# Performance work log

Measured on AMD Instinct MI355X. Metric: run time of the kernel, lower is better.

The kernel has to match this reference:

```python
import jax, jax.numpy as jnp
import numpy as np

NUM_GRAPHS = 8
NEG_SLOPE = 0.2


def add_self_loops(edge_index, n):
    loops = jnp.arange(n, dtype=edge_index.dtype)
    src = jnp.concatenate([edge_index[0], loops])
    dst = jnp.concatenate([edge_index[1], loops])
    return src, dst


def gat_conv(x, src, dst, W, att_src, att_dst, bias, concat):
    # x: [N, F_in]; W: [F_in, H*C]; att_src/att_dst: [H, C]; bias: [H*C] or [C]
    n = x.shape[0]
    H, C = att_src.shape
    xl = (x @ W).reshape(n, H, C)                     # [N, H, C]
    a_src = jnp.einsum('nhc,hc->nh', xl, att_src)     # [N, H]
    a_dst = jnp.einsum('nhc,hc->nh', xl, att_dst)     # [N, H]
    e = jax.nn.leaky_relu(a_src[src] + a_dst[dst], NEG_SLOPE)  # [E, H]
    # segment softmax over edges grouped by destination node
    m = jax.ops.segment_max(e, dst, num_segments=n)   # [N, H]
    e = jnp.exp(e - m[dst])
    denom = jax.ops.segment_sum(e, dst, num_segments=n)
    alpha = e / (denom[dst] + 1e-16)                  # [E, H]
    msg = xl[src] * alpha[:, :, None]                 # [E, H, C]
    out = jax.ops.segment_sum(msg, dst, num_segments=n)  # [N, H, C]
    out = out.reshape(n, H * C) if concat else out.mean(axis=1)
    return out + bias


def global_mean_pool(x, batch, num_graphs):
    s = jax.ops.segment_sum(x, batch, num_segments=num_graphs)
    cnt = jax.ops.segment_sum(jnp.ones((x.shape[0],), x.dtype), batch, num_segments=num_graphs)
    return s / jnp.maximum(cnt, 1.0)[:, None]


def setup_inputs() -> dict:
    key = jax.random.key(0)
    ks = jax.random.split(key, 12)
    N, E, F_in, Ch, H, F_out = 50000, 800000, 128, 64, 4, 128
    x = jax.random.normal(ks[0], (N, F_in), dtype=jnp.float32)
    edge_index = jax.random.randint(ks[1], (2, E), 0, N, dtype=jnp.int64)
    batch = jnp.sort(jax.random.randint(ks[2], (N,), 0, NUM_GRAPHS, dtype=jnp.int64))
    s = 0.1
    W1 = jax.random.normal(ks[3], (F_in, H * Ch), dtype=jnp.float32) * s
    att_src1 = jax.random.normal(ks[4], (H, Ch), dtype=jnp.float32) * s
    att_dst1 = jax.random.normal(ks[5], (H, Ch), dtype=jnp.float32) * s
    bias1 = jnp.zeros((H * Ch,), dtype=jnp.float32)
    W2 = jax.random.normal(ks[6], (H * Ch, F_out), dtype=jnp.float32) * s
    att_src2 = jax.random.normal(ks[7], (1, F_out), dtype=jnp.float32) * s
    att_dst2 = jax.random.normal(ks[8], (1, F_out), dtype=jnp.float32) * s
    bias2 = jnp.zeros((F_out,), dtype=jnp.float32)
    return {"x": x, "edge_index": edge_index, "batch": batch,
            "W1": W1, "att_src1": att_src1, "att_dst1": att_dst1, "bias1": bias1,
            "W2": W2, "att_src2": att_src2, "att_dst2": att_dst2, "bias2": bias2}


def reference(x, edge_index, batch, W1, att_src1, att_dst1, bias1, W2, att_src2, att_dst2, bias2):
    n = x.shape[0]
    src, dst = add_self_loops(edge_index, n)
    h = gat_conv(x, src, dst, W1, att_src1, att_dst1, bias1, concat=True)
    h = jax.nn.relu(h)
    h = gat_conv(h, src, dst, W2, att_src2, att_dst2, bias2, concat=False)
    return global_mean_pool(h, batch, NUM_GRAPHS)
```

## Files before the change

kernel.cpp:

```cpp
#include <hip/hip_runtime.h>
#include <cstdint>
#include <cstddef>

#define NEG_SLOPE 0.2f
#define LOG2E 1.44269504088896f
#define NREP 64

typedef __attribute__((ext_vector_type(8))) short bf16x8;
typedef __attribute__((ext_vector_type(4))) float f32x4;
typedef __attribute__((ext_vector_type(2))) float f32x2;

__device__ __forceinline__ ushort f2b(float f) {
  unsigned u = __float_as_uint(f);
  return (ushort)((u + 0x7FFFu + ((u >> 16) & 1)) >> 16);
}
__device__ __forceinline__ float fexp2(float x) {
#if __has_builtin(__builtin_amdgcn_exp2f)
  return __builtin_amdgcn_exp2f(x);
#else
  return __exp2f(x);
#endif
}
__device__ __forceinline__ int lbound(const int* __restrict__ a, int n, int key) {
  int lo = 0, hi = n;
  while (lo < hi) { int m = (lo + hi) >> 1; if (a[m] < key) lo = m + 1; else hi = m; }
  return lo;
}

__global__ __launch_bounds__(256) void setup_k(const float* __restrict__ W1,
                                               ushort* __restrict__ Bp1,
                                               const float* __restrict__ W2,
                                               ushort* __restrict__ Bp2,
                                               int* __restrict__ hist,
                                               float* __restrict__ pp, int n) {
  int i = blockIdx.x * 256 + threadIdx.x;
  {
    int k = i >> 8, c = i & 255;
    Bp1[(((size_t)(k >> 3) * 256 + c) << 3) + (k & 7)] = f2b(W1[i]);
  }
  {
    int k = i >> 7, c = i & 127;
    Bp2[(((size_t)(k >> 3) * 128 + c) << 3) + (k & 7)] = f2b(W2[i]);
  }
  if (i < n) hist[i] = 0;
  int i2 = i + 32768;
  if (i2 < n) hist[i2] = 0;
  pp[i] = 0.f;
  pp[i + 32768] = 0.f;
}

template<int N, int K, int C, int H, bool AF32>
__device__ __forceinline__ void gemm_attn_body(const void* __restrict__ A_,
                                               const ushort* __restrict__ Bp,
                                               const float* __restrict__ att_src,
                                               const float* __restrict__ att_dst,
                                               unsigned char* __restrict__ C8,
                                               float* __restrict__ a_src,
                                               float* __restrict__ a_dst,
                                               int M, int bid) {
  const int wave = threadIdx.x >> 6;
  const int lane = threadIdx.x & 63;
  const int strips = M / 16;
  const int strip = bid * 4 + wave;
  if (strip >= strips) return;
  const int r = lane & 15, kg = lane >> 4;
  const int row = strip * 16 + r;

  bf16x8 a[K / 32];
  if constexpr (AF32) {
    const float* Af = (const float*)A_;
    #pragma unroll
    for (int k0 = 0; k0 < K / 32; ++k0) {
      float4 f0 = *(const float4*)(Af + (size_t)row * K + k0 * 32 + kg * 8);
      float4 f1 = *(const float4*)(Af + (size_t)row * K + k0 * 32 + kg * 8 + 4);
      bf16x8 t;
      t[0] = (short)f2b(f0.x); t[1] = (short)f2b(f0.y);
      t[2] = (short)f2b(f0.z); t[3] = (short)f2b(f0.w);
      t[4] = (short)f2b(f1.x); t[5] = (short)f2b(f1.y);
      t[6] = (short)f2b(f1.z); t[7] = (short)f2b(f1.w);
      a[k0] = t;
    }
  } else {
    const ushort* Ab = (const ushort*)A_;
    #pragma unroll
    for (int k0 = 0; k0 < K / 32; ++k0)
      a[k0] = *(const bf16x8*)(Ab + (size_t)row * K + k0 * 32 + kg * 8);
  }

  float as_part[4] = {}, ad_part[4] = {};
  #pragma unroll 2
  for (int n0 = 0; n0 < N / 16; ++n0) {
    f32x4 acc = {0.f, 0.f, 0.f, 0.f};
    #pragma unroll
    for (int k0 = 0; k0 < K / 32; ++k0) {
      bf16x8 b = *(const bf16x8*)(Bp + ((size_t)(k0 * 4 + kg) * N + n0 * 16 + r) * 8);
      acc = __builtin_amdgcn_mfma_f32_16x16x32_bf16(a[k0], b, acc, 0, 0, 0);
    }
    float asv = att_src[n0 * 16 + r] * LOG2E;
    float adv = att_dst[n0 * 16 + r] * LOG2E;
    #pragma unroll
    for (int i = 0; i < 4; ++i) {
      as_part[i] = fmaf(acc[i], asv, as_part[i]);
      ad_part[i] = fmaf(acc[i], adv, ad_part[i]);
    }
    #pragma unroll
    for (int i = 0; i < 4; ++i) {
      int pk = __builtin_amdgcn_cvt_pk_fp8_f32(acc[i], acc[i], 0, false);
      C8[((size_t)strip * 16 + kg * 4 + i) * N + n0 * 16 + r] = (unsigned char)(pk & 0xFF);
    }
    if (((n0 + 1) * 16) % C == 0) {
      int h = (n0 * 16) / C;
      #pragma unroll
      for (int i = 0; i < 4; ++i) {
        float ts = as_part[i], td = ad_part[i];
        #pragma unroll
        for (int off = 1; off < 16; off <<= 1) {
          ts += __shfl_xor(ts, off);
          td += __shfl_xor(td, off);
        }
        if (r == i) {
          a_src[(size_t)(strip * 16 + kg * 4 + i) * H + h] = ts;
          a_dst[(size_t)(strip * 16 + kg * 4 + i) * H + h] = td;
        }
        as_part[i] = 0.f;
        ad_part[i] = 0.f;
      }
    }
  }
}

template<int N, int K, int C, int H, bool AF32>
__global__ __launch_bounds__(256) void gemm_rank_k(const void* __restrict__ A_,
                                                   const ushort* __restrict__ Bp,
                                                   const float* __restrict__ att_src,
                                                   const float* __restrict__ att_dst,
                                                   unsigned char* __restrict__ C8,
                                                   float* __restrict__ a_src,
                                                   float* __restrict__ a_dst, int M,
                                                   const int* __restrict__ edst,
                                                   int* __restrict__ hist,
                                                   int* __restrict__ rank,
                                                   int E, int GB) {
  if ((int)blockIdx.x < GB) {
    gemm_attn_body<N, K, C, H, AF32>(A_, Bp, att_src, att_dst, C8, a_src, a_dst,
                                     M, blockIdx.x);
  } else {
    int base = ((blockIdx.x - GB) * 256 + threadIdx.x) * 8;
    #pragma unroll
    for (int u = 0; u < 8; ++u) {
      int e = base + u;
      if (e < E) rank[e] = atomicAdd(hist + edst[e], 1);
    }
  }
}

template<int N, int K, int C, int H, bool AF32>
__global__ __launch_bounds__(256) void gemm_attn_k(const void* __restrict__ A_,
                                                   const ushort* __restrict__ Bp,
                                                   const float* __restrict__ att_src,
                                                   const float* __restrict__ att_dst,
                                                   unsigned char* __restrict__ C8,
                                                   float* __restrict__ a_src,
                                                   float* __restrict__ a_dst, int M) {
  gemm_attn_body<N, K, C, H, AF32>(A_, Bp, att_src, att_dst, C8, a_src, a_dst,
                                   M, blockIdx.x);
}

__global__ __launch_bounds__(256) void scan1_k(const int* __restrict__ hist,
                                               int* __restrict__ excl,
                                               int* __restrict__ chunksum, int n) {
  __shared__ int sums[256];
  int base = blockIdx.x * 1024 + threadIdx.x * 4;
  int4 v = {0, 0, 0, 0};
  if (base + 3 < n) v = *(const int4*)(hist + base);
  else {
    if (base < n)     v.x = hist[base];
    if (base + 1 < n) v.y = hist[base + 1];
    if (base + 2 < n) v.z = hist[base + 2];
    if (base + 3 < n) v.w = hist[base + 3];
  }
  int s = v.x + v.y + v.z + v.w;
  sums[threadIdx.x] = s;
  __syncthreads();
  for (int off = 1; off < 256; off <<= 1) {
    int t = (threadIdx.x >= (unsigned)off) ? sums[threadIdx.x - off] : 0;
    __syncthreads();
    sums[threadIdx.x] += t;
    __syncthreads();
  }
  if (threadIdx.x == 255) chunksum[blockIdx.x] = sums[255];
  int e0 = sums[threadIdx.x] - s;
  int e1 = e0 + v.x, e2 = e1 + v.y, e3 = e2 + v.z;
  if (base + 3 < n) {
    int4 o = {e0, e1, e2, e3};
    *(int4*)(excl + base) = o;
  } else {
    if (base < n)     excl[base] = e0;
    if (base + 1 < n) excl[base + 1] = e1;
    if (base + 2 < n) excl[base + 2] = e2;
    if (base + 3 < n) excl[base + 3] = e3;
  }
}

__global__ void scan2_k(const int* __restrict__ chunksum,
                        int* __restrict__ chunkoff, int nchunks) {
  if (threadIdx.x == 0) {
    int run = 0;
    for (int c = 0; c < nchunks; ++c) { chunkoff[c] = run; run += chunksum[c]; }
  }
}

__global__ __launch_bounds__(256) void addoff_k(int* __restrict__ rowptr,
                                                const int* __restrict__ chunkoff,
                                                int n, int total) {
  int i = blockIdx.x * 256 + threadIdx.x;
  if (i == 0) rowptr[n] = total;
  if (i >= n) return;
  rowptr[i] += chunkoff[i >> 10];
}

__global__ __launch_bounds__(256) void fill_k(const int* __restrict__ esrc,
                                              const int* __restrict__ edst,
                                              const int* __restrict__ rowptr,
                                              const int* __restrict__ rank,
                                              int* __restrict__ csr_src,
                                              int E, int Epad) {
  int e = blockIdx.x * 256 + threadIdx.x;
  if (e < E) csr_src[rowptr[edst[e]] + rank[e]] = esrc[e];
  else if (e < Epad) csr_src[e] = 0;
}

template<int H, int C>
__global__ __launch_bounds__(256) void agg1_k(const int* __restrict__ rowptr,
                                              const int* __restrict__ csr,
                                              const float* __restrict__ a_src,
                                              const float* __restrict__ a_dst,
                                              const unsigned char* __restrict__ xl,
                                              const float* __restrict__ bias,
                                              ushort* __restrict__ out, int n) {
  constexpr int F = H * C;
  const int wid0 = (blockIdx.x * 256 + threadIdx.x) >> 6;
  if (wid0 >= n) return;
  const int wid = __builtin_amdgcn_readfirstlane(wid0);
  const int lane = threadIdx.x & 63;
  const int h = lane >> 4;
  const uint lofs = (uint)lane * 4;
  const int j4 = lane & 3;
  const int je = lane >> 2;
  const int beg = rowptr[wid];
  const int end = rowptr[wid + 1];

  const float adh_s = a_dst[(uint)wid * 4 + j4];
  float vs_s = a_src[(uint)wid * 4 + j4] + adh_s;
  vs_s = fmaxf(vs_s, NEG_SLOPE * vs_s);

  float den = 1.f;
  float acc[4];
  {
    uint xs = *(const uint*)(xl + ((uint)wid * F + lofs));
    f32x2 lo = __builtin_amdgcn_cvt_pk_f32_fp8(xs, false);
    f32x2 hi = __builtin_amdgcn_cvt_pk_f32_fp8(xs, true);
    acc[0] = lo[0]; acc[1] = lo[1]; acc[2] = hi[0]; acc[3] = hi[1];
  }

  for (int j = beg; j < end; j += 16) {
    int sl = csr[j + je];
    float t = a_src[(uint)sl * 4 + j4] + adh_s;
    t = fmaxf(t, NEG_SLOPE * t);
    t = (j + je < end) ? t - vs_s : -1e30f;
    float pl = fexp2(t);
    uint xv[16];
    #pragma unroll
    for (int u = 0; u < 16; ++u) {
      int su = csr[j + u];
      xv[u] = *(const uint*)(xl + ((uint)su * F + lofs));
    }
    #pragma unroll
    for (int u = 0; u < 16; ++u) {
      float pu = __shfl(pl, u * 4 + h);
      den += pu;
      f32x2 lo = __builtin_amdgcn_cvt_pk_f32_fp8(xv[u], false);
      f32x2 hi = __builtin_amdgcn_cvt_pk_f32_fp8(xv[u], true);
      acc[0] = fmaf(pu, lo[0], acc[0]);
      acc[1] = fmaf(pu, lo[1], acc[1]);
      acc[2] = fmaf(pu, hi[0], acc[2]);
      acc[3] = fmaf(pu, hi[1], acc[3]);
    }
  }

  float inv = 1.f / (den + 1e-16f);
  float o[4];
  #pragma unroll
  for (int i = 0; i < 4; ++i)
    o[i] = fmaxf(fmaf(acc[i], inv, bias[lane * 4 + i]), 0.f);
  ushort4 ov = {f2b(o[0]), f2b(o[1]), f2b(o[2]), f2b(o[3])};
  *(ushort4*)(out + (size_t)wid * F + lane * 4) = ov;
}

__global__ __launch_bounds__(256) void agg2pool_k(const int* __restrict__ rowptr,
                                                  const int* __restrict__ csr,
                                                  const float* __restrict__ a_src,
                                                  const float* __restrict__ a_dst,
                                                  const unsigned char* __restrict__ xl,
                                                  const int* __restrict__ batch,
                                                  float* __restrict__ pp,
                                                  int n, int Emax) {
  const int pair = (blockIdx.x * 256 + threadIdx.x) >> 6;
  const int lane = threadIdx.x & 63;
  const int l32 = lane & 31;
  const int half = lane >> 5;
  int wid = pair * 2 + half;
  const bool act = wid < n;
  if (!act) wid = n - 1;
  const uint lofs = (uint)l32 * 4;
  const int beg = rowptr[wid];
  const int deg = rowptr[wid + 1] - beg;
  const int mdeg = max(deg, __shfl_xor(deg, 32));
  const float adh = a_dst[wid];

  float vs = a_src[wid] + adh;
  vs = fmaxf(vs, NEG_SLOPE * vs);
  float den = 1.f;
  float acc[4];
  {
    uint xs = *(const uint*)(xl + ((uint)wid * 128 + lofs));
    f32x2 lo = __builtin_amdgcn_cvt_pk_f32_fp8(xs, false);
    f32x2 hi = __builtin_amdgcn_cvt_pk_f32_fp8(xs, true);
    acc[0] = lo[0]; acc[1] = lo[1]; acc[2] = hi[0]; acc[3] = hi[1];
  }

  for (int j = 0; j < mdeg; j += 32) {
    int sl = csr[min(beg + j + l32, Emax)];
    float t = a_src[sl] + adh;
    t = fmaxf(t, NEG_SLOPE * t);
    t = (j + l32 < deg) ? t - vs : -1e30f;
    float pl = fexp2(t);
    #pragma unroll
    for (int g = 0; g < 2; ++g) {
      int su[16];
      uint xv[16];
      #pragma unroll
      for (int u = 0; u < 16; ++u) {
        su[u] = __shfl(sl, half * 32 + g * 16 + u);
        xv[u] = *(const uint*)(xl + ((uint)su[u] * 128 + lofs));
      }
      #pragma unroll
      for (int u = 0; u < 16; ++u) {
        float pu = __shfl(pl, half * 32 + g * 16 + u);
        den += pu;
        f32x2 lo = __builtin_amdgcn_cvt_pk_f32_fp8(xv[u], false);
        f32x2 hi = __builtin_amdgcn_cvt_pk_f32_fp8(xv[u], true);
        acc[0] = fmaf(pu, lo[0], acc[0]);
        acc[1] = fmaf(pu, lo[1], acc[1]);
        acc[2] = fmaf(pu, hi[0], acc[2]);
        acc[3] = fmaf(pu, hi[1], acc[3]);
      }
    }
  }

  __shared__ float red[8][128];
  __shared__ int gids[8];
  const int rrow = (threadIdx.x >> 6) * 2 + half;
  float inv = act ? 1.f / (den + 1e-16f) : 0.f;
  float4 ov = {acc[0] * inv, acc[1] * inv, acc[2] * inv, acc[3] * inv};
  *(float4*)&red[rrow][l32 * 4] = ov;
  if (l32 == 0) gids[rrow] = act ? batch[wid] : -1;
  __syncthreads();
  if (threadIdx.x < 128) {
    const int ch = threadIdx.x;
    float* base = pp + (size_t)(blockIdx.x & (NREP - 1)) * 8 * 128;
    float sum = 0.f;
    int cur = gids[0];
    #pragma unroll
    for (int r = 0; r < 8; ++r) {
      int g = gids[r];
      if (g != cur) {
        if (cur >= 0) unsafeAtomicAdd(base + cur * 128 + ch, sum);
        sum = 0.f;
        cur = g;
      }
      if (g >= 0) sum += red[r][ch];
    }
    if (cur >= 0) unsafeAtomicAdd(base + cur * 128 + ch, sum);
  }
}

__global__ __launch_bounds__(256) void finalize_k(const float* __restrict__ pp,
                                                  const int* __restrict__ batch,
                                                  const float* __restrict__ bias2,
                                                  float* __restrict__ out, int n) {
  int t = blockIdx.x * 256 + threadIdx.x;
  if (t >= 8 * 128) return;
  int g = t >> 7, c = t & 127;
  float s = 0.f;
  #pragma unroll 8
  for (int rep = 0; rep < NREP; ++rep) s += pp[rep * 8 * 128 + t];
  int lo = lbound(batch, n, g);
  int hi = lbound(batch, n, g + 1);
  float cnt = (float)(hi - lo);
  out[t] = s / fmaxf(cnt, 1.f) + bias2[c];
}

extern "C" void kernel_launch(void* const* d_in, const int* in_sizes, int n_in,
                              void* d_out, int out_size, void* d_ws, size_t ws_size,
                              hipStream_t stream) {
  const float* x        = (const float*)d_in[0];
  const int*   ei       = (const int*)d_in[1];
  const int*   batch    = (const int*)d_in[2];
  const float* W1       = (const float*)d_in[3];
  const float* att_src1 = (const float*)d_in[4];
  const float* att_dst1 = (const float*)d_in[5];
  const float* bias1    = (const float*)d_in[6];
  const float* W2       = (const float*)d_in[7];
  const float* att_src2 = (const float*)d_in[8];
  const float* att_dst2 = (const float*)d_in[9];
  const float* bias2    = (const float*)d_in[10];
  float* out = (float*)d_out;

  const int E  = in_sizes[1] / 2;
  const int NN = in_sizes[2];
  const int* esrc = ei;
  const int* edst = ei + E;
  const int PAD = 64;

  char* w = (char*)d_ws;
  size_t woff = 0;
  auto walloc = [&](size_t bytes) -> char* {
    char* r = w + woff;
    woff += (bytes + 255) & ~(size_t)255;
    return r;
  };
  unsigned char* xl1 = (unsigned char*)walloc((size_t)NN * 256);
  ushort* h1     = (ushort*)walloc((size_t)NN * 256 * 2);
  unsigned char* xl2 = (unsigned char*)walloc((size_t)NN * 128);
  float*  a_src1 = (float*)walloc((size_t)NN * 4 * 4);
  float*  a_dst1 = (float*)walloc((size_t)NN * 4 * 4);
  float*  a_src2 = (float*)walloc((size_t)NN * 4);
  float*  a_dst2 = (float*)walloc((size_t)NN * 4);
  int*    rowptr = (int*)walloc((size_t)(NN + 1) * 4);
  int*    hist   = (int*)walloc((size_t)NN * 4);
  int*    rank   = (int*)walloc((size_t)E * 4);
  int*    csrsrc = (int*)walloc((size_t)(E + PAD) * 4);
  ushort* Bp1    = (ushort*)walloc(128 * 256 * 2);
  ushort* Bp2    = (ushort*)walloc(256 * 128 * 2);
  int*    chunks = (int*)walloc(256 * 4);
  int*    chunko = (int*)walloc(256 * 4);
  float*  pp     = (float*)walloc((size_t)NREP * 8 * 128 * 4);

  dim3 blk(256);
  const int nbEp = (E + PAD + 255) / 256;
  const int nbN4 = (NN + 3) / 4;
  const int nbP  = ((NN + 1) / 2 + 3) / 4;
  const int gblocks = (NN / 16 + 3) / 4;
  const int rankBlocks = (E + 2047) / 2048;
  const int nchunks = (NN + 1023) / 1024;

  setup_k<<<128, blk, 0, stream>>>(W1, Bp1, W2, Bp2, hist, pp, NN);

  gemm_rank_k<256, 128, 64, 4, true><<<gblocks + rankBlocks, blk, 0, stream>>>(
      x, Bp1, att_src1, att_dst1, xl1, a_src1, a_dst1, NN,
      edst, hist, rank, E, gblocks);

  scan1_k<<<nchunks, blk, 0, stream>>>(hist, rowptr, chunks, NN);
  scan2_k<<<1, 64, 0, stream>>>(chunks, chunko, nchunks);
  addoff_k<<<(NN + 255) / 256, blk, 0, stream>>>(rowptr, chunko, NN, E);

  fill_k<<<nbEp, blk, 0, stream>>>(esrc, edst, rowptr, rank, csrsrc, E, E + PAD);

  agg1_k<4, 64><<<nbN4, blk, 0, stream>>>(
      rowptr, csrsrc, a_src1, a_dst1, xl1, bias1, h1, NN);

  gemm_attn_k<128, 256, 128, 1, false><<<gblocks, blk, 0, stream>>>(
      h1, Bp2, att_src2, att_dst2, xl2, a_src2, a_dst2, NN);

  agg2pool_k<<<nbP, blk, 0, stream>>>(
      rowptr, csrsrc, a_src2, a_dst2, xl2, batch, pp, NN, E + PAD - 1);

  finalize_k<<<4, blk, 0, stream>>>(pp, batch, bias2, out, NN);
}
```

Baseline: 162.3 us.

## Split GEMM column tiles across two waves and store FP8 output via LDS transpose

Each 16-row strip is now handled by two waves, each computing half of the output column tiles, which doubles the number of GEMM blocks. The FP8 results are transposed through shared memory so each lane writes a packed 4-byte word instead of single bytes. For layer 2 the two waves write partial attention logits, which the aggregation kernel reads as float2 and sums. The aim is more parallelism and fewer, wider stores, at the cost of extra LDS traffic and a doubled attention-logit buffer for layer 2.

```diff
diff --git a/kernel.cpp b/kernel.cpp
--- a/kernel.cpp
+++ b/kernel.cpp
@@ -49,7 +49,7 @@
   pp[i + 32768] = 0.f;
 }
 
-template<int N, int K, int C, int H, bool AF32>
+template<int N, int K, int C, int H, bool AF32, bool PARTIAL>
 __device__ __forceinline__ void gemm_attn_body(const void* __restrict__ A_,
                                                const ushort* __restrict__ Bp,
                                                const float* __restrict__ att_src,
@@ -58,13 +58,19 @@
                                                float* __restrict__ a_src,
                                                float* __restrict__ a_dst,
                                                int M, int bid) {
+  constexpr int T = N / 16;
+  constexpr int TH = T / 2;
+  __shared__ float tile[4][16][20];
   const int wave = threadIdx.x >> 6;
   const int lane = threadIdx.x & 63;
   const int strips = M / 16;
-  const int strip = bid * 4 + wave;
+  const int strip = bid * 2 + (wave >> 1);
+  const int half = wave & 1;
   if (strip >= strips) return;
   const int r = lane & 15, kg = lane >> 4;
   const int row = strip * 16 + r;
+  const int rt = kg * 4 + (r & 3);
+  const int cg = r >> 2;
 
   bf16x8 a[K / 32];
   if constexpr (AF32) {
@@ -88,8 +94,9 @@
   }
 
   float as_part[4] = {}, ad_part[4] = {};
-  #pragma unroll 2
-  for (int n0 = 0; n0 < N / 16; ++n0) {
+  #pragma unroll
+  for (int t = 0; t < TH; ++t) {
+    const int n0 = half * TH + t;
     f32x4 acc = {0.f, 0.f, 0.f, 0.f};
     #pragma unroll
     for (int k0 = 0; k0 < K / 32; ++k0) {
@@ -104,26 +111,46 @@
       ad_part[i] = fmaf(acc[i], adv, ad_part[i]);
     }
     #pragma unroll
+    for (int i = 0; i < 4; ++i) tile[wave][kg * 4 + i][r] = acc[i];
+    asm volatile("s_waitcnt lgkmcnt(0)" ::: "memory");
+    float4 tv = *(const float4*)&tile[wave][rt][cg * 4];
+    int dw = __builtin_amdgcn_cvt_pk_fp8_f32(tv.x, tv.y, 0, false);
+    dw = __builtin_amdgcn_cvt_pk_fp8_f32(tv.z, tv.w, dw, true);
+    *(unsigned*)(C8 + (size_t)(strip * 16 + rt) * N + (uint)(n0 * 16 + cg * 4)) =
+        (unsigned)dw;
+    if constexpr (!PARTIAL) {
+      if (((n0 + 1) * 16) % C == 0) {
+        int h = (n0 * 16) / C;
+        #pragma unroll
+        for (int i = 0; i < 4; ++i) {
+          float ts = as_part[i], td = ad_part[i];
+          #pragma unroll
+          for (int off = 1; off < 16; off <<= 1) {
+            ts += __shfl_xor(ts, off);
+            td += __shfl_xor(td, off);
+          }
+          if (r == i) {
+            a_src[(size_t)(strip * 16 + kg * 4 + i) * H + h] = ts;
+            a_dst[(size_t)(strip * 16 + kg * 4 + i) * H + h] = td;
+          }
+          as_part[i] = 0.f;
+          ad_part[i] = 0.f;
+        }
+      }
+    }
+  }
+  if constexpr (PARTIAL) {
+    #pragma unroll
     for (int i = 0; i < 4; ++i) {
-      int pk = __builtin_amdgcn_cvt_pk_fp8_f32(acc[i], acc[i], 0, false);
-      C8[((size_t)strip * 16 + kg * 4 + i) * N + n0 * 16 + r] = (unsigned char)(pk & 0xFF);
-    }
-    if (((n0 + 1) * 16) % C == 0) {
-      int h = (n0 * 16) / C;
+      float ts = as_part[i], td = ad_part[i];
       #pragma unroll
-      for (int i = 0; i < 4; ++i) {
-        float ts = as_part[i], td = ad_part[i];
-        #pragma unroll
-        for (int off = 1; off < 16; off <<= 1) {
-          ts += __shfl_xor(ts, off);
-          td += __shfl_xor(td, off);
-        }
-        if (r == i) {
-          a_src[(size_t)(strip * 16 + kg * 4 + i) * H + h] = ts;
-          a_dst[(size_t)(strip * 16 + kg * 4 + i) * H + h] = td;
-        }
-        as_part[i] = 0.f;
-        ad_part[i] = 0.f;
+      for (int off = 1; off < 16; off <<= 1) {
+        ts += __shfl_xor(ts, off);
+        td += __shfl_xor(td, off);
+      }
+      if (r == i) {
+        a_src[(size_t)(strip * 16 + kg * 4 + i) * 2 + half] = ts;
+        a_dst[(size_t)(strip * 16 + kg * 4 + i) * 2 + half] = td;
       }
     }
   }
@@ -142,8 +169,8 @@
                                                    int* __restrict__ rank,
                                                    int E, int GB) {
   if ((int)blockIdx.x < GB) {
-    gemm_attn_body<N, K, C, H, AF32>(A_, Bp, att_src, att_dst, C8, a_src, a_dst,
-                                     M, blockIdx.x);
+    gemm_attn_body<N, K, C, H, AF32, false>(A_, Bp, att_src, att_dst, C8,
+                                            a_src, a_dst, M, blockIdx.x);
   } else {
     int base = ((blockIdx.x - GB) * 256 + threadIdx.x) * 8;
     #pragma unroll
@@ -162,8 +189,8 @@
                                                    unsigned char* __restrict__ C8,
                                                    float* __restrict__ a_src,
                                                    float* __restrict__ a_dst, int M) {
-  gemm_attn_body<N, K, C, H, AF32>(A_, Bp, att_src, att_dst, C8, a_src, a_dst,
-                                   M, blockIdx.x);
+  gemm_attn_body<N, K, C, H, AF32, true>(A_, Bp, att_src, att_dst, C8,
+                                         a_src, a_dst, M, blockIdx.x);
 }
 
 __global__ __launch_bounds__(256) void scan1_k(const int* __restrict__ hist,
@@ -316,9 +343,11 @@
   const int beg = rowptr[wid];
   const int deg = rowptr[wid + 1] - beg;
   const int mdeg = max(deg, __shfl_xor(deg, 32));
-  const float adh = a_dst[wid];
-
-  float vs = a_src[wid] + adh;
+  const float2 ad2 = ((const float2*)a_dst)[wid];
+  const float adh = ad2.x + ad2.y;
+
+  float2 av2 = ((const float2*)a_src)[wid];
+  float vs = av2.x + av2.y + adh;
   vs = fmaxf(vs, NEG_SLOPE * vs);
   float den = 1.f;
   float acc[4];
@@ -331,7 +360,8 @@
 
   for (int j = 0; j < mdeg; j += 32) {
     int sl = csr[min(beg + j + l32, Emax)];
-    float t = a_src[sl] + adh;
+    float2 as2 = ((const float2*)a_src)[sl];
+    float t = as2.x + as2.y + adh;
     t = fmaxf(t, NEG_SLOPE * t);
     t = (j + l32 < deg) ? t - vs : -1e30f;
     float pl = fexp2(t);
@@ -435,8 +465,8 @@
   unsigned char* xl2 = (unsigned char*)walloc((size_t)NN * 128);
   float*  a_src1 = (float*)walloc((size_t)NN * 4 * 4);
   float*  a_dst1 = (float*)walloc((size_t)NN * 4 * 4);
-  float*  a_src2 = (float*)walloc((size_t)NN * 4);
-  float*  a_dst2 = (float*)walloc((size_t)NN * 4);
+  float*  a_src2 = (float*)walloc((size_t)NN * 2 * 4);
+  float*  a_dst2 = (float*)walloc((size_t)NN * 2 * 4);
   int*    rowptr = (int*)walloc((size_t)(NN + 1) * 4);
   int*    hist   = (int*)walloc((size_t)NN * 4);
   int*    rank   = (int*)walloc((size_t)E * 4);
@@ -451,7 +481,8 @@
   const int nbEp = (E + PAD + 255) / 256;
   const int nbN4 = (NN + 3) / 4;
   const int nbP  = ((NN + 1) / 2 + 3) / 4;
-  const int gblocks = (NN / 16 + 3) / 4;
+  const int strips = NN / 16;
+  const int gblocks = (strips * 2 + 3) / 4;
   const int rankBlocks = (E + 2047) / 2048;
   const int nchunks = (NN + 1023) / 1024;
 
```

After: 170.7 us. 5.2% more time.

## Stage packed weights in LDS and swap MFMA operands for row-contiguous output

Applied to the files above, without the earlier changes.

Each GEMM block now copies the packed bf16 weight matrix into shared memory with a rotation swizzle to avoid bank conflicts, and reads B fragments from LDS instead of global memory. The MFMA operands are swapped so each lane holds four consecutive output columns of one row. This lets the fp8 output be written as a packed 32-bit store and shortens the attention-score reduction to two cross-lane shuffles. The cost is 64 KB of shared memory per block, which limits occupancy, plus a full weight copy and a barrier in every block.

```diff
diff --git a/kernel.cpp b/kernel.cpp
--- a/kernel.cpp
+++ b/kernel.cpp
@@ -58,21 +58,33 @@
                                                float* __restrict__ a_src,
                                                float* __restrict__ a_dst,
                                                int M, int bid) {
-  const int wave = threadIdx.x >> 6;
-  const int lane = threadIdx.x & 63;
+  constexpr int ROWS = K / 8;
+  __shared__ ushort Bl[ROWS * N * 8];
+  const int tid = threadIdx.x;
+  #pragma unroll
+  for (int it = 0; it < ROWS * N / 256; ++it) {
+    int id = it * 256 + tid;
+    int brow = id / N, c = id % N;
+    int cs = (c + 2 * brow) & (N - 1);
+    *(bf16x8*)&Bl[((size_t)brow * N + cs) * 8] = *(const bf16x8*)&Bp[(size_t)id * 8];
+  }
+  __syncthreads();
+
+  const int wave = tid >> 6;
+  const int lane = tid & 63;
   const int strips = M / 16;
   const int strip = bid * 4 + wave;
   if (strip >= strips) return;
   const int r = lane & 15, kg = lane >> 4;
-  const int row = strip * 16 + r;
+  const int nrow = strip * 16 + r;
 
   bf16x8 a[K / 32];
   if constexpr (AF32) {
     const float* Af = (const float*)A_;
     #pragma unroll
     for (int k0 = 0; k0 < K / 32; ++k0) {
-      float4 f0 = *(const float4*)(Af + (size_t)row * K + k0 * 32 + kg * 8);
-      float4 f1 = *(const float4*)(Af + (size_t)row * K + k0 * 32 + kg * 8 + 4);
+      float4 f0 = *(const float4*)(Af + (size_t)nrow * K + k0 * 32 + kg * 8);
+      float4 f1 = *(const float4*)(Af + (size_t)nrow * K + k0 * 32 + kg * 8 + 4);
       bf16x8 t;
       t[0] = (short)f2b(f0.x); t[1] = (short)f2b(f0.y);
       t[2] = (short)f2b(f0.z); t[3] = (short)f2b(f0.w);
@@ -84,47 +96,37 @@
     const ushort* Ab = (const ushort*)A_;
     #pragma unroll
     for (int k0 = 0; k0 < K / 32; ++k0)
-      a[k0] = *(const bf16x8*)(Ab + (size_t)row * K + k0 * 32 + kg * 8);
-  }
-
-  float as_part[4] = {}, ad_part[4] = {};
-  #pragma unroll 2
+      a[k0] = *(const bf16x8*)(Ab + (size_t)nrow * K + k0 * 32 + kg * 8);
+  }
+
+  float as_p = 0.f, ad_p = 0.f;
+  #pragma unroll
   for (int n0 = 0; n0 < N / 16; ++n0) {
     f32x4 acc = {0.f, 0.f, 0.f, 0.f};
     #pragma unroll
     for (int k0 = 0; k0 < K / 32; ++k0) {
-      bf16x8 b = *(const bf16x8*)(Bp + ((size_t)(k0 * 4 + kg) * N + n0 * 16 + r) * 8);
-      acc = __builtin_amdgcn_mfma_f32_16x16x32_bf16(a[k0], b, acc, 0, 0, 0);
-    }
-    float asv = att_src[n0 * 16 + r] * LOG2E;
-    float adv = att_dst[n0 * 16 + r] * LOG2E;
-    #pragma unroll
-    for (int i = 0; i < 4; ++i) {
-      as_part[i] = fmaf(acc[i], asv, as_part[i]);
-      ad_part[i] = fmaf(acc[i], adv, ad_part[i]);
-    }
-    #pragma unroll
-    for (int i = 0; i < 4; ++i) {
-      int pk = __builtin_amdgcn_cvt_pk_fp8_f32(acc[i], acc[i], 0, false);
-      C8[((size_t)strip * 16 + kg * 4 + i) * N + n0 * 16 + r] = (unsigned char)(pk & 0xFF);
-    }
+      int brow = k0 * 4 + kg;
+      int cs = (n0 * 16 + r + 2 * brow) & (N - 1);
+      bf16x8 b = *(const bf16x8*)&Bl[((size_t)brow * N + cs) * 8];
+      acc = __builtin_amdgcn_mfma_f32_16x16x32_bf16(b, a[k0], acc, 0, 0, 0);
+    }
+    float4 avs = *(const float4*)(att_src + n0 * 16 + kg * 4);
+    float4 avd = *(const float4*)(att_dst + n0 * 16 + kg * 4);
+    as_p += acc[0] * avs.x + acc[1] * avs.y + acc[2] * avs.z + acc[3] * avs.w;
+    ad_p += acc[0] * avd.x + acc[1] * avd.y + acc[2] * avd.z + acc[3] * avd.w;
+    int dw = __builtin_amdgcn_cvt_pk_fp8_f32(acc[0], acc[1], 0, false);
+    dw = __builtin_amdgcn_cvt_pk_fp8_f32(acc[2], acc[3], dw, true);
+    *(unsigned*)(C8 + (size_t)nrow * N + (uint)(n0 * 16 + kg * 4)) = (unsigned)dw;
     if (((n0 + 1) * 16) % C == 0) {
-      int h = (n0 * 16) / C;
-      #pragma unroll
-      for (int i = 0; i < 4; ++i) {
-        float ts = as_part[i], td = ad_part[i];
-        #pragma unroll
-        for (int off = 1; off < 16; off <<= 1) {
-          ts += __shfl_xor(ts, off);
-          td += __shfl_xor(td, off);
-        }
-        if (r == i) {
-          a_src[(size_t)(strip * 16 + kg * 4 + i) * H + h] = ts;
-          a_dst[(size_t)(strip * 16 + kg * 4 + i) * H + h] = td;
-        }
-        as_part[i] = 0.f;
-        ad_part[i] = 0.f;
+      float ts = as_p * LOG2E, td = ad_p * LOG2E;
+      ts += __shfl_xor(ts, 16); ts += __shfl_xor(ts, 32);
+      td += __shfl_xor(td, 16); td += __shfl_xor(td, 32);
+      if (kg == 0) {
+        int h = (n0 * 16) / C;
+        a_src[(size_t)nrow * H + h] = ts;
+        a_dst[(size_t)nrow * H + h] = td;
       }
+      as_p = 0.f; ad_p = 0.f;
     }
   }
 }
@@ -142,8 +144,8 @@
                                                    int* __restrict__ rank,
                                                    int E, int GB) {
   if ((int)blockIdx.x < GB) {
-    gemm_attn_body<N, K, C, H, AF32>(A_, Bp, att_src, att_dst, C8, a_src, a_dst,
-                                     M, blockIdx.x);
+    gemm_attn_body<N, K, C, H, AF32>(A_, Bp, att_src, att_dst, C8,
+                                     a_src, a_dst, M, blockIdx.x);
   } else {
     int base = ((blockIdx.x - GB) * 256 + threadIdx.x) * 8;
     #pragma unroll
@@ -162,8 +164,8 @@
                                                    unsigned char* __restrict__ C8,
                                                    float* __restrict__ a_src,
                                                    float* __restrict__ a_dst, int M) {
-  gemm_attn_body<N, K, C, H, AF32>(A_, Bp, att_src, att_dst, C8, a_src, a_dst,
-                                   M, blockIdx.x);
+  gemm_attn_body<N, K, C, H, AF32>(A_, Bp, att_src, att_dst, C8,
+                                   a_src, a_dst, M, blockIdx.x);
 }
 
 __global__ __launch_bounds__(256) void scan1_k(const int* __restrict__ hist,
@@ -451,7 +453,8 @@
   const int nbEp = (E + PAD + 255) / 256;
   const int nbN4 = (NN + 3) / 4;
   const int nbP  = ((NN + 1) / 2 + 3) / 4;
-  const int gblocks = (NN / 16 + 3) / 4;
+  const int strips = NN / 16;
+  const int gblocks = (strips + 3) / 4;
   const int rankBlocks = (E + 2047) / 2048;
   const int nchunks = (NN + 1023) / 1024;
 
```

New measurement: 164.4 us. About the same (+1.3%).
